# Kernel optimization log

Measured on AMD Instinct MI355X. Metric: run time of the kernel, lower is better.

Reference implementation:

```python
import jax, jax.numpy as jnp
import numpy as np

TAU = 1.0
NUM_CLASSES = 14
LOSS_WEIGHT = 1.0
KERNEL_SUM = 26.0  # 3x3x3 ones with center zeroed


def setup_inputs() -> dict:
    key = jax.random.key(0)
    k1, k2, k3 = jax.random.split(key, 3)
    B, C, H, W, D = 2, NUM_CLASSES, 96, 96, 96
    preds_S = jax.random.normal(k1, (B, C, H, W, D), dtype=jnp.float32)
    preds_T = jax.random.normal(k2, (B, C, H, W, D), dtype=jnp.float32)
    gt_labels = jax.random.randint(k3, (B, 1, H, W, D), 0, NUM_CLASSES, dtype=jnp.int64)
    return {"preds_S": preds_S, "preds_T": preds_T, "gt_labels": gt_labels}


def _boundary_masks(gt_labels):
    # gt_labels: [B,1,H,W,D] int -> boundary mask per (batch, class): [B, nc, H*W*D]
    B = gt_labels.shape[0]
    H, W, D = gt_labels.shape[2:]
    kernel = jnp.ones((1, 1, 3, 3, 3), jnp.float32).at[0, 0, 1, 1, 1].set(0.0)
    onehot = (gt_labels[:, 0, None, :, :, :] ==
              jnp.arange(NUM_CLASSES)[None, :, None, None, None]).astype(jnp.float32)  # [B,nc,H,W,D]
    x = onehot.reshape(B * NUM_CLASSES, 1, H, W, D)
    conv = jax.lax.conv_general_dilated(x, kernel, (1, 1, 1), 'SAME')  # NCHWD
    conv = conv.reshape(B, NUM_CLASSES, H * W * D)
    # boundary[conv==26]=0 ; boundary[conv>0]=1
    return jnp.where(conv == KERNEL_SUM, 0.0, jnp.where(conv > 0.0, 1.0, 0.0))


def reference(preds_S, preds_T, gt_labels):
    B, C = preds_S.shape[0], preds_S.shape[1]
    boundary = _boundary_masks(gt_labels)                      # [B, nc, P]
    S = preds_S.reshape(B, C, -1) / TAU                        # [B, C, P]
    T = preds_T.reshape(B, C, -1) / TAU
    logS = jax.nn.log_softmax(S, axis=1)
    pT = jax.nn.softmax(T, axis=1)
    # per-voxel KL summed over classes (softmax is over class dim, same for every cls loop)
    kl_pos = jnp.sum(pT * (jnp.log(pT) - logS), axis=1)        # [B, P]
    count = boundary.sum(axis=-1)                              # [B, nc] boundary voxels
    num = jnp.einsum('bkp,bp->bk', boundary, kl_pos)           # [B, nc]
    # F.kl_div default reduction='mean' divides by C * n_boundary elements
    loss_bk = jnp.where(count > 0.0, num / (C * count), 0.0)
    return LOSS_WEIGHT * loss_bk.sum()
```

## Files before the change

kernel.cpp:

```cpp
#include <hip/hip_runtime.h>

#define NC 14
#define DIM 96
#define PP (DIM*DIM*DIM)
#define VPT 8
#define VPB (256*VPT)
#define BLOCKS_PER_B (PP/VPB)

__global__ __launch_bounds__(256) void bkd_main(
    const float* __restrict__ S, const float* __restrict__ T,
    const int* __restrict__ lab,
    double* __restrict__ gnum, int* __restrict__ gcnt)
{
    const int tid = threadIdx.x;
    const unsigned bq = blockIdx.x;
    const unsigned b  = bq / BLOCKS_PER_B;
    const int p = (int)((bq - b * BLOCKS_PER_B) * VPB) + tid * VPT;
    const int d = p % DIM;
    const int t = p / DIM;
    const int w = t % DIM;
    const int h = t / DIM;

    const float* tp = T + (size_t)b * NC * PP + p;
    const float* sp = S + (size_t)b * NC * PP + p;

    float ZT[VPT], ZS[VPT], A[VPT];
#pragma unroll
    for (int i = 0; i < VPT; ++i) { ZT[i] = 0.f; ZS[i] = 0.f; A[i] = 0.f; }

    float4 t0 = *(const float4*)(tp);
    float4 t1 = *(const float4*)(tp + 4);
    float4 s0 = *(const float4*)(sp);
    float4 s1 = *(const float4*)(sp + 4);

#define CONSUME()                                                            \
    {                                                                        \
        const float tv[VPT] = {t0.x, t0.y, t0.z, t0.w, t1.x, t1.y, t1.z, t1.w}; \
        const float sv[VPT] = {s0.x, s0.y, s0.z, s0.w, s1.x, s1.y, s1.z, s1.w}; \
        _Pragma("unroll")                                                    \
        for (int i = 0; i < VPT; ++i) {                                      \
            const float u = __expf(tv[i]);                                   \
            ZT[i] += u;                                                      \
            ZS[i] += __expf(sv[i]);                                          \
            A[i]   = fmaf(u, tv[i] - sv[i], A[i]);                           \
        }                                                                    \
    }

#pragma unroll 1
    for (int c = 0; c < NC - 1; ++c) {
        const float* tpn = tp + PP;
        const float* spn = sp + PP;
        const float4 nt0 = *(const float4*)(tpn);
        const float4 nt1 = *(const float4*)(tpn + 4);
        const float4 ns0 = *(const float4*)(spn);
        const float4 ns1 = *(const float4*)(spn + 4);
        CONSUME();
        tp = tpn; sp = spn;
        t0 = nt0; t1 = nt1; s0 = ns0; s1 = ns1;
    }
    CONSUME();
#undef CONSUME

    float kl[VPT];
#pragma unroll
    for (int i = 0; i < VPT; ++i)
        kl[i] = A[i] / ZT[i] + __logf(ZS[i]) - __logf(ZT[i]);

    const int lbase = (int)b * PP;
    unsigned mk[VPT];
#pragma unroll
    for (int i = 0; i < VPT; ++i) mk[i] = 0u;

#pragma unroll
    for (int dh = -1; dh <= 1; ++dh) {
        const int hh = h + dh;
        if ((unsigned)hh >= (unsigned)DIM) continue;
#pragma unroll
        for (int dw = -1; dw <= 1; ++dw) {
            const int ww = w + dw;
            if ((unsigned)ww >= (unsigned)DIM) continue;
            const int* rp = lab + lbase + (hh * DIM + ww) * DIM + d;
            const int4 v0 = *(const int4*)rp;
            const int4 v1 = *(const int4*)(rp + 4);
            unsigned lb[VPT + 2];
            lb[0] = (d > 0)         ? (1u << rp[-1])  : 0u;
            lb[1] = 1u << v0.x;  lb[2] = 1u << v0.y;
            lb[3] = 1u << v0.z;  lb[4] = 1u << v0.w;
            lb[5] = 1u << v1.x;  lb[6] = 1u << v1.y;
            lb[7] = 1u << v1.z;  lb[8] = 1u << v1.w;
            lb[9] = (d < DIM - VPT) ? (1u << rp[VPT]) : 0u;
            if (dh == 0 && dw == 0) {
#pragma unroll
                for (int i = 0; i < VPT; ++i) mk[i] |= lb[i] | lb[i + 2];
            } else {
#pragma unroll
                for (int i = 0; i < VPT; ++i) mk[i] |= lb[i] | lb[i + 1] | lb[i + 2];
            }
        }
    }

    const bool hwi = (h >= 1 && h <= DIM - 2 && w >= 1 && w <= DIM - 2);
#pragma unroll
    for (int i = 0; i < VPT; ++i) {
        const int dd = d + i;
        const bool din = (dd > 0) && (dd < DIM - 1);
        if (hwi && din && (mk[i] & (mk[i] - 1)) == 0u) mk[i] = 0u;
    }

    float lnum[NC];
    int   lcnt[NC];
#pragma unroll
    for (int k = 0; k < NC; ++k) { lnum[k] = 0.f; lcnt[k] = 0; }
#pragma unroll
    for (int i = 0; i < VPT; ++i) {
        const float kv = kl[i];
        const unsigned mm = mk[i];
#pragma unroll
        for (int k = 0; k < NC; ++k) {
            lnum[k] += (mm & (1u << k)) ? kv : 0.f;
            lcnt[k] += (mm >> k) & 1u;
        }
    }

#pragma unroll
    for (int k = 0; k < NC; ++k) {
        float v = lnum[k];
        int   c = lcnt[k];
#pragma unroll
        for (int off = 32; off > 0; off >>= 1) {
            v += __shfl_down(v, off, 64);
            c += __shfl_down(c, off, 64);
        }
        lnum[k] = v; lcnt[k] = c;
    }

    __shared__ float s_num[NC];
    __shared__ int   s_cnt[NC];
    if (tid < NC) { s_num[tid] = 0.f; s_cnt[tid] = 0; }
    __syncthreads();
    if ((tid & 63) == 0) {
#pragma unroll
        for (int k = 0; k < NC; ++k) {
            atomicAdd(&s_num[k], lnum[k]);
            atomicAdd(&s_cnt[k], lcnt[k]);
        }
    }
    __syncthreads();
    if (tid < NC) {
        atomicAdd(&gnum[b * NC + tid], (double)s_num[tid]);
        atomicAdd(&gcnt[b * NC + tid], s_cnt[tid]);
    }
}

__global__ void bkd_final(const double* __restrict__ gnum,
                          const int* __restrict__ gcnt,
                          float* __restrict__ out)
{
    const int i = threadIdx.x;
    double term = 0.0;
    if (i < 2 * NC) {
        const int c = gcnt[i];
        if (c > 0) term = gnum[i] / ((double)NC * (double)c);
    }
#pragma unroll
    for (int off = 32; off > 0; off >>= 1)
        term += __shfl_down(term, off, 64);
    if (i == 0) out[0] = (float)term;
}

extern "C" void kernel_launch(void* const* d_in, const int* in_sizes, int n_in,
                              void* d_out, int out_size, void* d_ws, size_t ws_size,
                              hipStream_t stream) {
    const float* S  = (const float*)d_in[0];
    const float* T  = (const float*)d_in[1];
    const int* lab  = (const int*)d_in[2];
    float* out      = (float*)d_out;

    double* gnum = (double*)d_ws;
    int*    gcnt = (int*)((char*)d_ws + 2 * NC * sizeof(double));

    hipMemsetAsync(d_ws, 0, 2 * NC * (sizeof(double) + sizeof(int)), stream);

    bkd_main<<<2 * BLOCKS_PER_B, 256, 0, stream>>>(S, T, lab, gnum, gcnt);
    bkd_final<<<1, 64, 0, stream>>>(gnum, gcnt, out);
}
```

Baseline: 238.8 us.

## Split fused kernel into KL sweep and boundary-mask passes with deeper prefetch

Splits the single fused kernel in two. The first kernel computes the per-voxel KL and writes it to a workspace buffer, loading four classes ahead through a fully unrolled rotating register pipeline. The second kernel reads that KL buffer together with the labels, builds the boundary masks and reduces them. The aim is lower register pressure in each kernel and more memory-level parallelism in the streaming pass, at the cost of an extra launch and an extra write and read of a 2*96^3 float buffer. The original fused kernel is kept as a fallback for when the workspace is too small.

```diff
diff --git a/kernel.cpp b/kernel.cpp
--- a/kernel.cpp
+++ b/kernel.cpp
@@ -4,12 +4,82 @@
 #define DIM 96
 #define PP (DIM*DIM*DIM)
 #define VPT 8
-#define VPB (256*VPT)
+#define BS  256
+#define VPB (BS*VPT)
 #define BLOCKS_PER_B (PP/VPB)
 
-__global__ __launch_bounds__(256) void bkd_main(
+
+__global__ __launch_bounds__(BS) void bkd_sweep(
     const float* __restrict__ S, const float* __restrict__ T,
-    const int* __restrict__ lab,
+    float* __restrict__ klb)
+{
+    const int tid = threadIdx.x;
+    const unsigned bq = blockIdx.x;
+    const unsigned b  = bq / BLOCKS_PER_B;
+    const int p = (int)((bq - b * BLOCKS_PER_B) * VPB) + tid * VPT;
+
+    const float* tp = T + (size_t)b * NC * PP + p;
+    const float* sp = S + (size_t)b * NC * PP + p;
+
+    float ZT[VPT], ZS[VPT], A[VPT];
+#pragma unroll
+    for (int i = 0; i < VPT; ++i) { ZT[i] = 0.f; ZS[i] = 0.f; A[i] = 0.f; }
+
+    float4 Atl,Ath,Asl,Ash, Btl,Bth,Bsl,Bsh, Ctl,Cth,Csl,Csh, Dtl,Dth,Dsl,Dsh;
+
+#define LOADC(P, c)                                                          \
+    { const float* tq = tp + (size_t)(c) * PP;                               \
+      const float* sq = sp + (size_t)(c) * PP;                               \
+      P##tl = *(const float4*)tq; P##th = *(const float4*)(tq + 4);          \
+      P##sl = *(const float4*)sq; P##sh = *(const float4*)(sq + 4); }
+
+#define CONS(P)                                                              \
+    { const float tv[VPT] = {P##tl.x,P##tl.y,P##tl.z,P##tl.w,                \
+                             P##th.x,P##th.y,P##th.z,P##th.w};               \
+      const float sv[VPT] = {P##sl.x,P##sl.y,P##sl.z,P##sl.w,                \
+                             P##sh.x,P##sh.y,P##sh.z,P##sh.w};               \
+      _Pragma("unroll")                                                      \
+      for (int i = 0; i < VPT; ++i) {                                        \
+          const float u = __expf(tv[i]);                                     \
+          ZT[i] += u;                                                        \
+          ZS[i] += __expf(sv[i]);                                            \
+          A[i]   = fmaf(u, tv[i] - sv[i], A[i]); } }
+
+    LOADC(A,0)  LOADC(B,1)  LOADC(C,2)
+    LOADC(D,3)   CONS(A)
+    LOADC(A,4)   CONS(B)
+    LOADC(B,5)   CONS(C)
+    LOADC(C,6)   CONS(D)
+    LOADC(D,7)   CONS(A)
+    LOADC(A,8)   CONS(B)
+    LOADC(B,9)   CONS(C)
+    LOADC(C,10)  CONS(D)
+    LOADC(D,11)  CONS(A)
+    LOADC(A,12)  CONS(B)
+    LOADC(B,13)  CONS(C)
+    CONS(D)
+    CONS(A)
+    CONS(B)
+#undef LOADC
+#undef CONS
+
+    float4 k0, k1;
+    k0.x = A[0]/ZT[0] + __logf(ZS[0]) - __logf(ZT[0]);
+    k0.y = A[1]/ZT[1] + __logf(ZS[1]) - __logf(ZT[1]);
+    k0.z = A[2]/ZT[2] + __logf(ZS[2]) - __logf(ZT[2]);
+    k0.w = A[3]/ZT[3] + __logf(ZS[3]) - __logf(ZT[3]);
+    k1.x = A[4]/ZT[4] + __logf(ZS[4]) - __logf(ZT[4]);
+    k1.y = A[5]/ZT[5] + __logf(ZS[5]) - __logf(ZT[5]);
+    k1.z = A[6]/ZT[6] + __logf(ZS[6]) - __logf(ZT[6]);
+    k1.w = A[7]/ZT[7] + __logf(ZS[7]) - __logf(ZT[7]);
+
+    float* kp = klb + (size_t)b * PP + p;
+    *(float4*)kp       = k0;
+    *(float4*)(kp + 4) = k1;
+}
+
+__global__ __launch_bounds__(BS) void bkd_mask(
+    const float* __restrict__ klb, const int* __restrict__ lab,
     double* __restrict__ gnum, int* __restrict__ gcnt)
 {
     const int tid = threadIdx.x;
@@ -21,50 +91,10 @@
     const int w = t % DIM;
     const int h = t / DIM;
 
-    const float* tp = T + (size_t)b * NC * PP + p;
-    const float* sp = S + (size_t)b * NC * PP + p;
-
-    float ZT[VPT], ZS[VPT], A[VPT];
-#pragma unroll
-    for (int i = 0; i < VPT; ++i) { ZT[i] = 0.f; ZS[i] = 0.f; A[i] = 0.f; }
-
-    float4 t0 = *(const float4*)(tp);
-    float4 t1 = *(const float4*)(tp + 4);
-    float4 s0 = *(const float4*)(sp);
-    float4 s1 = *(const float4*)(sp + 4);
-
-#define CONSUME()                                                            \
-    {                                                                        \
-        const float tv[VPT] = {t0.x, t0.y, t0.z, t0.w, t1.x, t1.y, t1.z, t1.w}; \
-        const float sv[VPT] = {s0.x, s0.y, s0.z, s0.w, s1.x, s1.y, s1.z, s1.w}; \
-        _Pragma("unroll")                                                    \
-        for (int i = 0; i < VPT; ++i) {                                      \
-            const float u = __expf(tv[i]);                                   \
-            ZT[i] += u;                                                      \
-            ZS[i] += __expf(sv[i]);                                          \
-            A[i]   = fmaf(u, tv[i] - sv[i], A[i]);                           \
-        }                                                                    \
-    }
-
-#pragma unroll 1
-    for (int c = 0; c < NC - 1; ++c) {
-        const float* tpn = tp + PP;
-        const float* spn = sp + PP;
-        const float4 nt0 = *(const float4*)(tpn);
-        const float4 nt1 = *(const float4*)(tpn + 4);
-        const float4 ns0 = *(const float4*)(spn);
-        const float4 ns1 = *(const float4*)(spn + 4);
-        CONSUME();
-        tp = tpn; sp = spn;
-        t0 = nt0; t1 = nt1; s0 = ns0; s1 = ns1;
-    }
-    CONSUME();
-#undef CONSUME
-
-    float kl[VPT];
-#pragma unroll
-    for (int i = 0; i < VPT; ++i)
-        kl[i] = A[i] / ZT[i] + __logf(ZS[i]) - __logf(ZT[i]);
+    const float* kp = klb + (size_t)b * PP + p;
+    const float4 k0 = *(const float4*)kp;
+    const float4 k1 = *(const float4*)(kp + 4);
+    const float kl[VPT] = {k0.x,k0.y,k0.z,k0.w,k1.x,k1.y,k1.z,k1.w};
 
     const int lbase = (int)b * PP;
     unsigned mk[VPT];
@@ -152,6 +182,151 @@
     }
 }
 
+__global__ __launch_bounds__(BS) void bkd_fused(
+    const float* __restrict__ S, const float* __restrict__ T,
+    const int* __restrict__ lab,
+    double* __restrict__ gnum, int* __restrict__ gcnt)
+{
+    const int tid = threadIdx.x;
+    const unsigned bq = blockIdx.x;
+    const unsigned b  = bq / BLOCKS_PER_B;
+    const int p = (int)((bq - b * BLOCKS_PER_B) * VPB) + tid * VPT;
+    const int d = p % DIM;
+    const int t = p / DIM;
+    const int w = t % DIM;
+    const int h = t / DIM;
+
+    const float* tp = T + (size_t)b * NC * PP + p;
+    const float* sp = S + (size_t)b * NC * PP + p;
+
+    float ZT[VPT], ZS[VPT], A[VPT];
+#pragma unroll
+    for (int i = 0; i < VPT; ++i) { ZT[i] = 0.f; ZS[i] = 0.f; A[i] = 0.f; }
+
+    float4 t0 = *(const float4*)(tp);
+    float4 t1 = *(const float4*)(tp + 4);
+    float4 s0 = *(const float4*)(sp);
+    float4 s1 = *(const float4*)(sp + 4);
+
+#define CONSUME()                                                            \
+    {                                                                        \
+        const float tv[VPT] = {t0.x, t0.y, t0.z, t0.w, t1.x, t1.y, t1.z, t1.w}; \
+        const float sv[VPT] = {s0.x, s0.y, s0.z, s0.w, s1.x, s1.y, s1.z, s1.w}; \
+        _Pragma("unroll")                                                    \
+        for (int i = 0; i < VPT; ++i) {                                      \
+            const float u = __expf(tv[i]);                                   \
+            ZT[i] += u;                                                      \
+            ZS[i] += __expf(sv[i]);                                          \
+            A[i]   = fmaf(u, tv[i] - sv[i], A[i]);                           \
+        }                                                                    \
+    }
+
+#pragma unroll 1
+    for (int c = 0; c < NC - 1; ++c) {
+        const float* tpn = tp + PP;
+        const float* spn = sp + PP;
+        const float4 nt0 = *(const float4*)(tpn);
+        const float4 nt1 = *(const float4*)(tpn + 4);
+        const float4 ns0 = *(const float4*)(spn);
+        const float4 ns1 = *(const float4*)(spn + 4);
+        CONSUME();
+        tp = tpn; sp = spn;
+        t0 = nt0; t1 = nt1; s0 = ns0; s1 = ns1;
+    }
+    CONSUME();
+#undef CONSUME
+
+    float kl[VPT];
+#pragma unroll
+    for (int i = 0; i < VPT; ++i)
+        kl[i] = A[i] / ZT[i] + __logf(ZS[i]) - __logf(ZT[i]);
+
+    const int lbase = (int)b * PP;
+    unsigned mk[VPT];
+#pragma unroll
+    for (int i = 0; i < VPT; ++i) mk[i] = 0u;
+
+#pragma unroll
+    for (int dh = -1; dh <= 1; ++dh) {
+        const int hh = h + dh;
+        if ((unsigned)hh >= (unsigned)DIM) continue;
+#pragma unroll
+        for (int dw = -1; dw <= 1; ++dw) {
+            const int ww = w + dw;
+            if ((unsigned)ww >= (unsigned)DIM) continue;
+            const int* rp = lab + lbase + (hh * DIM + ww) * DIM + d;
+            const int4 v0 = *(const int4*)rp;
+            const int4 v1 = *(const int4*)(rp + 4);
+            unsigned lb[VPT + 2];
+            lb[0] = (d > 0)         ? (1u << rp[-1])  : 0u;
+            lb[1] = 1u << v0.x;  lb[2] = 1u << v0.y;
+            lb[3] = 1u << v0.z;  lb[4] = 1u << v0.w;
+            lb[5] = 1u << v1.x;  lb[6] = 1u << v1.y;
+            lb[7] = 1u << v1.z;  lb[8] = 1u << v1.w;
+            lb[9] = (d < DIM - VPT) ? (1u << rp[VPT]) : 0u;
+            if (dh == 0 && dw == 0) {
+#pragma unroll
+                for (int i = 0; i < VPT; ++i) mk[i] |= lb[i] | lb[i + 2];
+            } else {
+#pragma unroll
+                for (int i = 0; i < VPT; ++i) mk[i] |= lb[i] | lb[i + 1] | lb[i + 2];
+            }
+        }
+    }
+
+    const bool hwi = (h >= 1 && h <= DIM - 2 && w >= 1 && w <= DIM - 2);
+#pragma unroll
+    for (int i = 0; i < VPT; ++i) {
+        const int dd = d + i;
+        const bool din = (dd > 0) && (dd < DIM - 1);
+        if (hwi && din && (mk[i] & (mk[i] - 1)) == 0u) mk[i] = 0u;
+    }
+
+    float lnum[NC];
+    int   lcnt[NC];
+#pragma unroll
+    for (int k = 0; k < NC; ++k) { lnum[k] = 0.f; lcnt[k] = 0; }
+#pragma unroll
+    for (int i = 0; i < VPT; ++i) {
+        const float kv = kl[i];
+        const unsigned mm = mk[i];
+#pragma unroll
+        for (int k = 0; k < NC; ++k) {
+            lnum[k] += (mm & (1u << k)) ? kv : 0.f;
+            lcnt[k] += (mm >> k) & 1u;
+        }
+    }
+
+#pragma unroll
+    for (int k = 0; k < NC; ++k) {
+        float v = lnum[k];
+        int   c = lcnt[k];
+#pragma unroll
+        for (int off = 32; off > 0; off >>= 1) {
+            v += __shfl_down(v, off, 64);
+            c += __shfl_down(c, off, 64);
+        }
+        lnum[k] = v; lcnt[k] = c;
+    }
+
+    __shared__ float s_num[NC];
+    __shared__ int   s_cnt[NC];
+    if (tid < NC) { s_num[tid] = 0.f; s_cnt[tid] = 0; }
+    __syncthreads();
+    if ((tid & 63) == 0) {
+#pragma unroll
+        for (int k = 0; k < NC; ++k) {
+            atomicAdd(&s_num[k], lnum[k]);
+            atomicAdd(&s_cnt[k], lcnt[k]);
+        }
+    }
+    __syncthreads();
+    if (tid < NC) {
+        atomicAdd(&gnum[b * NC + tid], (double)s_num[tid]);
+        atomicAdd(&gcnt[b * NC + tid], s_cnt[tid]);
+    }
+}
+
 __global__ void bkd_final(const double* __restrict__ gnum,
                           const int* __restrict__ gcnt,
                           float* __restrict__ out)
@@ -178,9 +353,17 @@
 
     double* gnum = (double*)d_ws;
     int*    gcnt = (int*)((char*)d_ws + 2 * NC * sizeof(double));
-
-    hipMemsetAsync(d_ws, 0, 2 * NC * (sizeof(double) + sizeof(int)), stream);
-
-    bkd_main<<<2 * BLOCKS_PER_B, 256, 0, stream>>>(S, T, lab, gnum, gcnt);
+    float*  klb  = (float*)((char*)d_ws + 1024);
+
+    const size_t need = 1024 + (size_t)2 * PP * sizeof(float);
+
+    hipMemsetAsync(d_ws, 0, 1024, stream);
+
+    if (ws_size >= need) {
+        bkd_sweep<<<2 * BLOCKS_PER_B, BS, 0, stream>>>(S, T, klb);
+        bkd_mask <<<2 * BLOCKS_PER_B, BS, 0, stream>>>(klb, lab, gnum, gcnt);
+    } else {
+        bkd_fused<<<2 * BLOCKS_PER_B, BS, 0, stream>>>(S, T, lab, gnum, gcnt);
+    }
     bkd_final<<<1, 64, 0, stream>>>(gnum, gcnt, out);
 }
```

Result: slower. 263.0 us (+10.1%).
